# Performance work log

Measured on AMD Instinct MI355X. Metric: run time of the kernel, lower is better.

The kernel has to match this reference:

```python
import jax, jax.numpy as jnp
import numpy as np


def setup_inputs() -> dict:
    key = jax.random.key(0)
    k1, k2, k3, k4 = jax.random.split(key, 4)
    B = 2_000_000
    T_STEPS = 8
    # Storages: positive, realistic magnitudes (mm)
    y = jax.random.uniform(k1, (B, 5), dtype=jnp.float32) * 100.0
    # Realistic HBV parameters:
    # tt, tti, ttm, cfr, cfmax, whc, cflux, fc, lp, beta, k0, alpha, perc, k1
    theta = jnp.array([0.0, 2.0, 0.0, 0.05, 3.0, 0.1, 1.0, 200.0, 0.7,
                       2.0, 0.2, 0.5, 2.0, 0.05], dtype=jnp.float32)
    # Climate: P (precip, mm/d), Ep (pot. evap, mm/d), T (temp, C)
    P = jax.random.uniform(k2, (T_STEPS, B, 1), dtype=jnp.float32) * 10.0
    Ep = jax.random.uniform(k3, (T_STEPS, B, 1), dtype=jnp.float32) * 5.0
    Tair = jax.random.normal(k4, (T_STEPS, B, 1), dtype=jnp.float32) * 10.0
    climate_data = jnp.concatenate([P, Ep, Tair], axis=2)
    delta_t = jnp.asarray(1.0, dtype=jnp.float32)
    t = 3
    return {"y": y, "theta": theta, "climate_data": climate_data,
            "delta_t": delta_t, "t": t}


def _hbv_rhs(y, theta, climate_t, dt):
    tt, tti, ttm, cfr, cfmax, whc, cflux, fc, lp, beta, k0, alpha, perc, k1 = \
        [theta[i] for i in range(14)]
    S1, S2, S3, S4, S5 = (y[:, i] for i in range(5))
    P, Ep, T = climate_t[:, 0], climate_t[:, 1], climate_t[:, 2]

    zero = jnp.float32(0.0)
    # snowfall_2
    flux_sf = jnp.minimum(P, jnp.maximum(zero, P * (tt + 0.5 * tti - T) / tti))
    # refreeze_1
    flux_refr = jnp.maximum(jnp.minimum(cfr * cfmax * (ttm - T), S2 / dt), zero)
    # melt_1
    flux_melt = jnp.maximum(jnp.minimum(cfmax * (T - ttm), S1 / dt), zero)
    # rainfall_2
    flux_rf = jnp.minimum(P, jnp.maximum(zero, P * (T - (tt - 0.5 * tti)) / tti))
    # infiltration_3 with smoothThreshold_storage_logistic(S2, whc*S1)
    r, e = jnp.float32(0.01), jnp.float32(5.0)
    Smax_raw = whc * S1
    Smax = jnp.maximum(Smax_raw, zero)
    logistic = 1.0 / (1.0 + jnp.exp((S2 - Smax + r * e * Smax) / jnp.maximum(r, r * Smax)))
    flux_in = (flux_rf + flux_melt) * (1.0 - logistic)
    # excess_1 (uses unclipped Smax_raw)
    flux_se = jnp.maximum((S2 - Smax_raw) / dt, zero)
    # capillary_1
    flux_cf = jnp.minimum(cflux * (1.0 - S3 / fc), S4 / dt)
    # evap_3: min over {S3/(lp*fc)*Ep, Ep, S3/dt}
    flux_ea = jnp.minimum(jnp.minimum(S3 / (lp * fc) * Ep, Ep), S3 / dt)
    # recharge_2
    flux_r = (flux_in + flux_se) * (jnp.maximum(S3, zero) / fc) ** beta
    # interflow_2
    flux_q0 = jnp.minimum(k0 * jnp.maximum(S4, zero) ** (1.0 + alpha),
                          jnp.maximum(S4 / dt, zero))
    # percolation_1
    flux_perc = jnp.minimum(perc, S4 / dt)
    # baseflow_1
    flux_q1 = k1 * S5

    dS = jnp.stack([
        flux_sf + flux_refr - flux_melt,
        flux_rf + flux_melt - flux_refr - flux_in - flux_se,
        flux_in + flux_se + flux_cf - flux_ea - flux_r,
        flux_r - flux_cf - flux_q0 - flux_perc,
        flux_perc - flux_q1,
    ], axis=1)
    fluxes = jnp.stack([
        flux_sf, flux_refr, flux_melt, flux_rf, flux_in, flux_se,
        flux_cf, flux_ea, flux_r, flux_q0, flux_perc, flux_q1,
    ], axis=1)
    return dS, fluxes


def reference(y, theta, climate_data, delta_t, t):
    climate_t = climate_data[t]  # [B, 3] -> P, Ep, T
    return _hbv_rhs(y, theta, climate_t, delta_t)
```

## Files before the change

kernel.cpp:

```cpp
#include <hip/hip_runtime.h>
#include <math.h>


__global__ __launch_bounds__(256) void hbv_rhs_kernel(
    const float* __restrict__ y,
    const float* __restrict__ theta,
    const float* __restrict__ climate,
    const float* __restrict__ dt_ptr,
    const int* __restrict__ t_ptr,
    float* __restrict__ dS,
    float* __restrict__ fluxes,
    int B)
{
    int i = blockIdx.x * blockDim.x + threadIdx.x;
    if (i >= B) return;

    const float tt    = theta[0];
    const float tti   = theta[1];
    const float ttm   = theta[2];
    const float cfr   = theta[3];
    const float cfmax = theta[4];
    const float whc   = theta[5];
    const float cflux = theta[6];
    const float fc    = theta[7];
    const float lp    = theta[8];
    const float beta  = theta[9];
    const float k0    = theta[10];
    const float alpha = theta[11];
    const float perc  = theta[12];
    const float k1    = theta[13];
    const float dt    = dt_ptr[0];
    const int   t     = t_ptr[0];

    const float* __restrict__ ct = climate + (size_t)t * (size_t)B * 3u;

    const size_t yb = (size_t)i * 5u;
    const float S1 = y[yb + 0];
    const float S2 = y[yb + 1];
    const float S3 = y[yb + 2];
    const float S4 = y[yb + 3];
    const float S5 = y[yb + 4];

    const size_t cb = (size_t)i * 3u;
    const float P  = ct[cb + 0];
    const float Ep = ct[cb + 1];
    const float T  = ct[cb + 2];

    const float zero = 0.0f;

    const float flux_sf   = fminf(P, fmaxf(zero, P * (tt + 0.5f * tti - T) / tti));
    const float flux_refr = fmaxf(fminf(cfr * cfmax * (ttm - T), S2 / dt), zero);
    const float flux_melt = fmaxf(fminf(cfmax * (T - ttm), S1 / dt), zero);
    const float flux_rf   = fminf(P, fmaxf(zero, P * (T - (tt - 0.5f * tti)) / tti));

    const float r = 0.01f, e = 5.0f;
    const float Smax_raw = whc * S1;
    const float Smax     = fmaxf(Smax_raw, zero);
    const float logistic = 1.0f / (1.0f + expf((S2 - Smax + r * e * Smax) / fmaxf(r, r * Smax)));
    const float flux_in  = (flux_rf + flux_melt) * (1.0f - logistic);
    const float flux_se  = fmaxf((S2 - Smax_raw) / dt, zero);
    const float flux_cf  = fminf(cflux * (1.0f - S3 / fc), S4 / dt);
    const float flux_ea  = fminf(fminf(S3 / (lp * fc) * Ep, Ep), S3 / dt);
    const float flux_r   = (flux_in + flux_se) * powf(fmaxf(S3, zero) / fc, beta);
    const float flux_q0  = fminf(k0 * powf(fmaxf(S4, zero), 1.0f + alpha), fmaxf(S4 / dt, zero));
    const float flux_perc = fminf(perc, S4 / dt);
    const float flux_q1  = k1 * S5;

    const size_t db = (size_t)i * 5u;
    dS[db + 0] = flux_sf + flux_refr - flux_melt;
    dS[db + 1] = flux_rf + flux_melt - flux_refr - flux_in - flux_se;
    dS[db + 2] = flux_in + flux_se + flux_cf - flux_ea - flux_r;
    dS[db + 3] = flux_r - flux_cf - flux_q0 - flux_perc;
    dS[db + 4] = flux_perc - flux_q1;

    float4* __restrict__ frow = (float4*)(fluxes + (size_t)i * 12u);
    frow[0] = make_float4(flux_sf, flux_refr, flux_melt, flux_rf);
    frow[1] = make_float4(flux_in, flux_se, flux_cf, flux_ea);
    frow[2] = make_float4(flux_r, flux_q0, flux_perc, flux_q1);
}

extern "C" void kernel_launch(void* const* d_in, const int* in_sizes, int n_in,
                              void* d_out, int out_size, void* d_ws, size_t ws_size,
                              hipStream_t stream) {
    const float* y       = (const float*)d_in[0];
    const float* theta   = (const float*)d_in[1];
    const float* climate = (const float*)d_in[2];
    const float* dt_ptr  = (const float*)d_in[3];
    const int*   t_ptr   = (const int*)d_in[4];

    const int B = in_sizes[0] / 5;

    float* dS     = (float*)d_out;
    float* fluxes = (float*)d_out + (size_t)B * 5u;

    const int block = 256;
    const int grid  = (B + block - 1) / block;
    hbv_rhs_kernel<<<grid, block, 0, stream>>>(y, theta, climate, dt_ptr, t_ptr,
                                               dS, fluxes, B);
}
```

Measured before the change: 301.0 us.

## Stage strided row loads and stores through LDS for coalesced float4 access

Loads each block's contiguous y and climate slices into shared memory with coalesced float4 reads, computes fluxes from LDS, then writes dS and fluxes back through LDS with coalesced float4 stores. The goal is to replace per-thread stride-5, stride-3 and stride-12 global accesses with fully coalesced vector transactions in this memory-bound kernel. It adds two block barriers, LDS bank conflicts from the strided LDS indexing, and about 25 KB of LDS per block, which may limit occupancy. Float4 casts assume base offsets stay 16-byte aligned, which holds because block size is a multiple of 4.

```diff
diff --git a/kernel.cpp b/kernel.cpp
--- a/kernel.cpp
+++ b/kernel.cpp
@@ -2,7 +2,9 @@
 #include <math.h>
 
 
-__global__ __launch_bounds__(256) void hbv_rhs_kernel(
+#define BLOCK 256
+
+__global__ __launch_bounds__(BLOCK) void hbv_rhs_kernel(
     const float* __restrict__ y,
     const float* __restrict__ theta,
     const float* __restrict__ climate,
@@ -12,8 +14,32 @@
     float* __restrict__ fluxes,
     int B)
 {
-    int i = blockIdx.x * blockDim.x + threadIdx.x;
-    if (i >= B) return;
+    __shared__ float lds_y[BLOCK * 5];
+    __shared__ float lds_c[BLOCK * 3];
+    __shared__ float lds_d[BLOCK * 5];
+    __shared__ float lds_f[BLOCK * 12];
+
+    const int tid  = threadIdx.x;
+    const int base = blockIdx.x * BLOCK;
+    if (base >= B) return;
+    const int nrows = min(BLOCK, B - base);
+
+    const float dt = dt_ptr[0];
+    const int   t  = t_ptr[0];
+    const float* __restrict__ ct = climate + (size_t)t * (size_t)B * 3u;
+
+    const float* __restrict__ yb = y  + (size_t)base * 5u;
+    const float* __restrict__ cb = ct + (size_t)base * 3u;
+    const int ny = nrows * 5, nc = nrows * 3;
+    const int ny4 = ny >> 2, nc4 = nc >> 2;
+    for (int k = tid; k < ny4; k += BLOCK)
+        ((float4*)lds_y)[k] = ((const float4*)yb)[k];
+    for (int k = ny4 * 4 + tid; k < ny; k += BLOCK)
+        lds_y[k] = yb[k];
+    for (int k = tid; k < nc4; k += BLOCK)
+        ((float4*)lds_c)[k] = ((const float4*)cb)[k];
+    for (int k = nc4 * 4 + tid; k < nc; k += BLOCK)
+        lds_c[k] = cb[k];
 
     const float tt    = theta[0];
     const float tti   = theta[1];
@@ -29,54 +55,64 @@
     const float alpha = theta[11];
     const float perc  = theta[12];
     const float k1    = theta[13];
-    const float dt    = dt_ptr[0];
-    const int   t     = t_ptr[0];
 
-    const float* __restrict__ ct = climate + (size_t)t * (size_t)B * 3u;
+    __syncthreads();
 
-    const size_t yb = (size_t)i * 5u;
-    const float S1 = y[yb + 0];
-    const float S2 = y[yb + 1];
-    const float S3 = y[yb + 2];
-    const float S4 = y[yb + 3];
-    const float S5 = y[yb + 4];
+    if (tid < nrows) {
+        const float S1 = lds_y[tid * 5 + 0];
+        const float S2 = lds_y[tid * 5 + 1];
+        const float S3 = lds_y[tid * 5 + 2];
+        const float S4 = lds_y[tid * 5 + 3];
+        const float S5 = lds_y[tid * 5 + 4];
+        const float P  = lds_c[tid * 3 + 0];
+        const float Ep = lds_c[tid * 3 + 1];
+        const float T  = lds_c[tid * 3 + 2];
 
-    const size_t cb = (size_t)i * 3u;
-    const float P  = ct[cb + 0];
-    const float Ep = ct[cb + 1];
-    const float T  = ct[cb + 2];
+        const float zero = 0.0f;
+        const float flux_sf   = fminf(P, fmaxf(zero, P * (tt + 0.5f * tti - T) / tti));
+        const float flux_refr = fmaxf(fminf(cfr * cfmax * (ttm - T), S2 / dt), zero);
+        const float flux_melt = fmaxf(fminf(cfmax * (T - ttm), S1 / dt), zero);
+        const float flux_rf   = fminf(P, fmaxf(zero, P * (T - (tt - 0.5f * tti)) / tti));
 
-    const float zero = 0.0f;
+        const float r = 0.01f, e = 5.0f;
+        const float Smax_raw = whc * S1;
+        const float Smax     = fmaxf(Smax_raw, zero);
+        const float logistic = 1.0f / (1.0f + expf((S2 - Smax + r * e * Smax) / fmaxf(r, r * Smax)));
+        const float flux_in  = (flux_rf + flux_melt) * (1.0f - logistic);
+        const float flux_se  = fmaxf((S2 - Smax_raw) / dt, zero);
+        const float flux_cf  = fminf(cflux * (1.0f - S3 / fc), S4 / dt);
+        const float flux_ea  = fminf(fminf(S3 / (lp * fc) * Ep, Ep), S3 / dt);
+        const float flux_r   = (flux_in + flux_se) * powf(fmaxf(S3, zero) / fc, beta);
+        const float flux_q0  = fminf(k0 * powf(fmaxf(S4, zero), 1.0f + alpha), fmaxf(S4 / dt, zero));
+        const float flux_perc = fminf(perc, S4 / dt);
+        const float flux_q1  = k1 * S5;
 
-    const float flux_sf   = fminf(P, fmaxf(zero, P * (tt + 0.5f * tti - T) / tti));
-    const float flux_refr = fmaxf(fminf(cfr * cfmax * (ttm - T), S2 / dt), zero);
-    const float flux_melt = fmaxf(fminf(cfmax * (T - ttm), S1 / dt), zero);
-    const float flux_rf   = fminf(P, fmaxf(zero, P * (T - (tt - 0.5f * tti)) / tti));
+        lds_d[tid * 5 + 0] = flux_sf + flux_refr - flux_melt;
+        lds_d[tid * 5 + 1] = flux_rf + flux_melt - flux_refr - flux_in - flux_se;
+        lds_d[tid * 5 + 2] = flux_in + flux_se + flux_cf - flux_ea - flux_r;
+        lds_d[tid * 5 + 3] = flux_r - flux_cf - flux_q0 - flux_perc;
+        lds_d[tid * 5 + 4] = flux_perc - flux_q1;
 
-    const float r = 0.01f, e = 5.0f;
-    const float Smax_raw = whc * S1;
-    const float Smax     = fmaxf(Smax_raw, zero);
-    const float logistic = 1.0f / (1.0f + expf((S2 - Smax + r * e * Smax) / fmaxf(r, r * Smax)));
-    const float flux_in  = (flux_rf + flux_melt) * (1.0f - logistic);
-    const float flux_se  = fmaxf((S2 - Smax_raw) / dt, zero);
-    const float flux_cf  = fminf(cflux * (1.0f - S3 / fc), S4 / dt);
-    const float flux_ea  = fminf(fminf(S3 / (lp * fc) * Ep, Ep), S3 / dt);
-    const float flux_r   = (flux_in + flux_se) * powf(fmaxf(S3, zero) / fc, beta);
-    const float flux_q0  = fminf(k0 * powf(fmaxf(S4, zero), 1.0f + alpha), fmaxf(S4 / dt, zero));
-    const float flux_perc = fminf(perc, S4 / dt);
-    const float flux_q1  = k1 * S5;
+        float4* f4 = (float4*)(lds_f + tid * 12);
+        f4[0] = make_float4(flux_sf, flux_refr, flux_melt, flux_rf);
+        f4[1] = make_float4(flux_in, flux_se, flux_cf, flux_ea);
+        f4[2] = make_float4(flux_r, flux_q0, flux_perc, flux_q1);
+    }
 
-    const size_t db = (size_t)i * 5u;
-    dS[db + 0] = flux_sf + flux_refr - flux_melt;
-    dS[db + 1] = flux_rf + flux_melt - flux_refr - flux_in - flux_se;
-    dS[db + 2] = flux_in + flux_se + flux_cf - flux_ea - flux_r;
-    dS[db + 3] = flux_r - flux_cf - flux_q0 - flux_perc;
-    dS[db + 4] = flux_perc - flux_q1;
+    __syncthreads();
 
-    float4* __restrict__ frow = (float4*)(fluxes + (size_t)i * 12u);
-    frow[0] = make_float4(flux_sf, flux_refr, flux_melt, flux_rf);
-    frow[1] = make_float4(flux_in, flux_se, flux_cf, flux_ea);
-    frow[2] = make_float4(flux_r, flux_q0, flux_perc, flux_q1);
+    float* __restrict__ db = dS     + (size_t)base * 5u;
+    float* __restrict__ fb = fluxes + (size_t)base * 12u;
+    const int nd = nrows * 5, nf = nrows * 12;
+    const int nd4 = nd >> 2, nf4 = nf >> 2;
+    for (int k = tid; k < nd4; k += BLOCK)
+        ((float4*)db)[k] = ((const float4*)lds_d)[k];
+    for (int k = nd4 * 4 + tid; k < nd; k += BLOCK)
+        db[k] = lds_d[k];
+    for (int k = tid; k < nf4; k += BLOCK)
+        ((float4*)fb)[k] = ((const float4*)lds_f)[k];
+    for (int k = nf4 * 4 + tid; k < nf; k += BLOCK)
+        fb[k] = lds_f[k];
 }
 
 extern "C" void kernel_launch(void* const* d_in, const int* in_sizes, int n_in,
@@ -93,7 +129,7 @@
     float* dS     = (float*)d_out;
     float* fluxes = (float*)d_out + (size_t)B * 5u;
 
-    const int block = 256;
+    const int block = BLOCK;
     const int grid  = (B + block - 1) / block;
     hbv_rhs_kernel<<<grid, block, 0, stream>>>(y, theta, climate, dt_ptr, t_ptr,
                                                dS, fluxes, B);
```

After: 295.3 us. Within noise of the previous version (-1.9%).

## Process four rows per thread with 16-byte vector loads and nontemporal stores

Applied to the files above, without the earlier changes.

Each thread now handles four consecutive rows. Their 20 state floats and 12 climate floats are loaded as aligned float4 vectors, and all outputs are written as float4 nontemporal stores. Before, the scalar stride-5 and stride-3 loads and the stride-5 dS stores were poorly coalesced. The change raises register pressure and cuts the thread count by four, and vector alignment relies on the group offsets being multiples of 16 bytes, with a scalar tail path for leftover rows.

```diff
diff --git a/kernel.cpp b/kernel.cpp
--- a/kernel.cpp
+++ b/kernel.cpp
@@ -2,7 +2,52 @@
 #include <math.h>
 
 
-__global__ __launch_bounds__(256) void hbv_rhs_kernel(
+#define BLOCK 256
+
+typedef float nfloat4 __attribute__((ext_vector_type(4)));
+
+struct HbvParams {
+    float tt, tti, ttm, cfr, cfmax, whc, cflux, fc, lp, beta, k0, alpha, perc, k1, dt;
+};
+
+__device__ __forceinline__ void hbv_row(const float S1, const float S2, const float S3,
+                                        const float S4, const float S5,
+                                        const float P, const float Ep, const float T,
+                                        const HbvParams& p,
+                                        float* __restrict__ d,
+                                        float* __restrict__ f)
+{
+    const float zero = 0.0f;
+    const float flux_sf   = fminf(P, fmaxf(zero, P * (p.tt + 0.5f * p.tti - T) / p.tti));
+    const float flux_refr = fmaxf(fminf(p.cfr * p.cfmax * (p.ttm - T), S2 / p.dt), zero);
+    const float flux_melt = fmaxf(fminf(p.cfmax * (T - p.ttm), S1 / p.dt), zero);
+    const float flux_rf   = fminf(P, fmaxf(zero, P * (T - (p.tt - 0.5f * p.tti)) / p.tti));
+
+    const float r = 0.01f, e = 5.0f;
+    const float Smax_raw = p.whc * S1;
+    const float Smax     = fmaxf(Smax_raw, zero);
+    const float logistic = 1.0f / (1.0f + expf((S2 - Smax + r * e * Smax) / fmaxf(r, r * Smax)));
+    const float flux_in  = (flux_rf + flux_melt) * (1.0f - logistic);
+    const float flux_se  = fmaxf((S2 - Smax_raw) / p.dt, zero);
+    const float flux_cf  = fminf(p.cflux * (1.0f - S3 / p.fc), S4 / p.dt);
+    const float flux_ea  = fminf(fminf(S3 / (p.lp * p.fc) * Ep, Ep), S3 / p.dt);
+    const float flux_r   = (flux_in + flux_se) * powf(fmaxf(S3, zero) / p.fc, p.beta);
+    const float flux_q0  = fminf(p.k0 * powf(fmaxf(S4, zero), 1.0f + p.alpha), fmaxf(S4 / p.dt, zero));
+    const float flux_perc = fminf(p.perc, S4 / p.dt);
+    const float flux_q1  = p.k1 * S5;
+
+    d[0] = flux_sf + flux_refr - flux_melt;
+    d[1] = flux_rf + flux_melt - flux_refr - flux_in - flux_se;
+    d[2] = flux_in + flux_se + flux_cf - flux_ea - flux_r;
+    d[3] = flux_r - flux_cf - flux_q0 - flux_perc;
+    d[4] = flux_perc - flux_q1;
+
+    f[0] = flux_sf;  f[1] = flux_refr; f[2] = flux_melt; f[3] = flux_rf;
+    f[4] = flux_in;  f[5] = flux_se;   f[6] = flux_cf;   f[7] = flux_ea;
+    f[8] = flux_r;   f[9] = flux_q0;   f[10] = flux_perc; f[11] = flux_q1;
+}
+
+__global__ __launch_bounds__(BLOCK) void hbv_rhs_kernel(
     const float* __restrict__ y,
     const float* __restrict__ theta,
     const float* __restrict__ climate,
@@ -12,71 +57,71 @@
     float* __restrict__ fluxes,
     int B)
 {
-    int i = blockIdx.x * blockDim.x + threadIdx.x;
-    if (i >= B) return;
+    const int j = blockIdx.x * blockDim.x + threadIdx.x;
+    const int r0 = j * 4;
+    if (r0 >= B) return;
 
-    const float tt    = theta[0];
-    const float tti   = theta[1];
-    const float ttm   = theta[2];
-    const float cfr   = theta[3];
-    const float cfmax = theta[4];
-    const float whc   = theta[5];
-    const float cflux = theta[6];
-    const float fc    = theta[7];
-    const float lp    = theta[8];
-    const float beta  = theta[9];
-    const float k0    = theta[10];
-    const float alpha = theta[11];
-    const float perc  = theta[12];
-    const float k1    = theta[13];
-    const float dt    = dt_ptr[0];
-    const int   t     = t_ptr[0];
-
+    HbvParams p;
+    p.tt    = theta[0];  p.tti   = theta[1];  p.ttm   = theta[2];
+    p.cfr   = theta[3];  p.cfmax = theta[4];  p.whc   = theta[5];
+    p.cflux = theta[6];  p.fc    = theta[7];  p.lp    = theta[8];
+    p.beta  = theta[9];  p.k0    = theta[10]; p.alpha = theta[11];
+    p.perc  = theta[12]; p.k1    = theta[13];
+    p.dt    = dt_ptr[0];
+    const int t = t_ptr[0];
     const float* __restrict__ ct = climate + (size_t)t * (size_t)B * 3u;
 
-    const size_t yb = (size_t)i * 5u;
-    const float S1 = y[yb + 0];
-    const float S2 = y[yb + 1];
-    const float S3 = y[yb + 2];
-    const float S4 = y[yb + 3];
-    const float S5 = y[yb + 4];
+    if (r0 + 3 < B) {
+        const nfloat4* __restrict__ y4 = (const nfloat4*)(y  + (size_t)j * 20u);
+        const nfloat4* __restrict__ c4 = (const nfloat4*)(ct + (size_t)j * 12u);
+        nfloat4 a0 = y4[0], a1 = y4[1], a2 = y4[2], a3 = y4[3], a4 = y4[4];
+        nfloat4 c0 = c4[0], c1 = c4[1], c2 = c4[2];
 
-    const size_t cb = (size_t)i * 3u;
-    const float P  = ct[cb + 0];
-    const float Ep = ct[cb + 1];
-    const float T  = ct[cb + 2];
+        float S[4][5] = {
+            { a0.x, a0.y, a0.z, a0.w, a1.x },
+            { a1.y, a1.z, a1.w, a2.x, a2.y },
+            { a2.z, a2.w, a3.x, a3.y, a3.z },
+            { a3.w, a4.x, a4.y, a4.z, a4.w }
+        };
+        float C[4][3] = {
+            { c0.x, c0.y, c0.z },
+            { c0.w, c1.x, c1.y },
+            { c1.z, c1.w, c2.x },
+            { c2.y, c2.z, c2.w }
+        };
 
-    const float zero = 0.0f;
+        float d[4][5], f[4][12];
+        #pragma unroll
+        for (int k = 0; k < 4; ++k)
+            hbv_row(S[k][0], S[k][1], S[k][2], S[k][3], S[k][4],
+                    C[k][0], C[k][1], C[k][2], p, d[k], f[k]);
 
-    const float flux_sf   = fminf(P, fmaxf(zero, P * (tt + 0.5f * tti - T) / tti));
-    const float flux_refr = fmaxf(fminf(cfr * cfmax * (ttm - T), S2 / dt), zero);
-    const float flux_melt = fmaxf(fminf(cfmax * (T - ttm), S1 / dt), zero);
-    const float flux_rf   = fminf(P, fmaxf(zero, P * (T - (tt - 0.5f * tti)) / tti));
+        nfloat4* __restrict__ d4 = (nfloat4*)(dS + (size_t)j * 20u);
+        const float* dd = &d[0][0];
+        #pragma unroll
+        for (int k = 0; k < 5; ++k) {
+            nfloat4 v = { dd[4*k], dd[4*k+1], dd[4*k+2], dd[4*k+3] };
+            __builtin_nontemporal_store(v, d4 + k);
+        }
 
-    const float r = 0.01f, e = 5.0f;
-    const float Smax_raw = whc * S1;
-    const float Smax     = fmaxf(Smax_raw, zero);
-    const float logistic = 1.0f / (1.0f + expf((S2 - Smax + r * e * Smax) / fmaxf(r, r * Smax)));
-    const float flux_in  = (flux_rf + flux_melt) * (1.0f - logistic);
-    const float flux_se  = fmaxf((S2 - Smax_raw) / dt, zero);
-    const float flux_cf  = fminf(cflux * (1.0f - S3 / fc), S4 / dt);
-    const float flux_ea  = fminf(fminf(S3 / (lp * fc) * Ep, Ep), S3 / dt);
-    const float flux_r   = (flux_in + flux_se) * powf(fmaxf(S3, zero) / fc, beta);
-    const float flux_q0  = fminf(k0 * powf(fmaxf(S4, zero), 1.0f + alpha), fmaxf(S4 / dt, zero));
-    const float flux_perc = fminf(perc, S4 / dt);
-    const float flux_q1  = k1 * S5;
-
-    const size_t db = (size_t)i * 5u;
-    dS[db + 0] = flux_sf + flux_refr - flux_melt;
-    dS[db + 1] = flux_rf + flux_melt - flux_refr - flux_in - flux_se;
-    dS[db + 2] = flux_in + flux_se + flux_cf - flux_ea - flux_r;
-    dS[db + 3] = flux_r - flux_cf - flux_q0 - flux_perc;
-    dS[db + 4] = flux_perc - flux_q1;
-
-    float4* __restrict__ frow = (float4*)(fluxes + (size_t)i * 12u);
-    frow[0] = make_float4(flux_sf, flux_refr, flux_melt, flux_rf);
-    frow[1] = make_float4(flux_in, flux_se, flux_cf, flux_ea);
-    frow[2] = make_float4(flux_r, flux_q0, flux_perc, flux_q1);
+        nfloat4* __restrict__ f4 = (nfloat4*)(fluxes + (size_t)j * 48u);
+        const float* ff = &f[0][0];
+        #pragma unroll
+        for (int k = 0; k < 12; ++k) {
+            nfloat4 v = { ff[4*k], ff[4*k+1], ff[4*k+2], ff[4*k+3] };
+            __builtin_nontemporal_store(v, f4 + k);
+        }
+    } else {
+        for (int rr = r0; rr < B; ++rr) {
+            const size_t yb = (size_t)rr * 5u;
+            const size_t cb = (size_t)rr * 3u;
+            float d[5], f[12];
+            hbv_row(y[yb], y[yb+1], y[yb+2], y[yb+3], y[yb+4],
+                    ct[cb], ct[cb+1], ct[cb+2], p, d, f);
+            for (int q = 0; q < 5; ++q)  dS[(size_t)rr * 5u + q] = d[q];
+            for (int q = 0; q < 12; ++q) fluxes[(size_t)rr * 12u + q] = f[q];
+        }
+    }
 }
 
 extern "C" void kernel_launch(void* const* d_in, const int* in_sizes, int n_in,
@@ -93,8 +138,8 @@
     float* dS     = (float*)d_out;
     float* fluxes = (float*)d_out + (size_t)B * 5u;
 
-    const int block = 256;
-    const int grid  = (B + block - 1) / block;
-    hbv_rhs_kernel<<<grid, block, 0, stream>>>(y, theta, climate, dt_ptr, t_ptr,
+    const int ngroups = (B + 3) / 4;
+    const int grid    = (ngroups + BLOCK - 1) / BLOCK;
+    hbv_rhs_kernel<<<grid, BLOCK, 0, stream>>>(y, theta, climate, dt_ptr, t_ptr,
                                                dS, fluxes, B);
 }
```

Measured after the change: 589.8 us. +96.0%, slower.
